# Kernel optimization log

Measured on AMD Instinct MI355X. Metric: run time of the kernel, lower is better.

Reference implementation:

```python
import jax, jax.numpy as jnp
import numpy as np

N = 102400      # total agents across all groups
GROUP = 50      # agents per group
G = N // GROUP  # 2048 groups
E = 128         # embedding_dim
H = 512         # h_dim


def setup_inputs() -> dict:
    key = jax.random.key(0)
    k1, k2, k3, k4, k5, k6 = jax.random.split(key, 6)
    hist_enc = jax.random.normal(k1, (N, H), dtype=jnp.float32)
    hist_pos_batch = jax.random.normal(k2, (N, 2), dtype=jnp.float32)
    # group boundaries: 0, 50, 100, ..., N  (len = G+1)
    seq_start_end = (jnp.arange(G + 1, dtype=jnp.int32) * GROUP)
    # spatial_embedding: Linear(2, E)
    Ws = jax.random.normal(k3, (2, E), dtype=jnp.float32) * (1.0 / np.sqrt(2.0))
    bs = jax.random.normal(k4, (E,), dtype=jnp.float32) * 0.01
    # mlp_pre_pool: Linear(E + H, H)
    Wm = jax.random.normal(k5, (E + H, H), dtype=jnp.float32) * (1.0 / np.sqrt(E + H))
    bm = jax.random.normal(k6, (H,), dtype=jnp.float32) * 0.01
    return {
        "hist_enc": hist_enc,
        "hist_pos_batch": hist_pos_batch,
        "seq_start_end": seq_start_end,
        "Ws": Ws, "bs": bs, "Wm": Wm, "bm": bm,
    }


def reference(hist_enc, hist_pos_batch, seq_start_end, Ws, bs, Wm, bm):
    # The original torch loop builds all n^2 pairs per group but keeps only
    # curr_pool_h[0:1], i.e. row i=0 -> pooled vector for the group's FIRST agent.
    # rel[i=0, j] = pos[j] - pos[start]; hidden index is j; max over j.
    n = hist_enc.shape[0]
    num_groups = seq_start_end.shape[0] - 1
    # segment id of each agent: group g covers [sse[g], sse[g+1])
    seg_ids = jnp.searchsorted(seq_start_end, jnp.arange(n, dtype=seq_start_end.dtype), side="right") - 1
    starts = seq_start_end[:-1]                      # [G]
    anchor = hist_pos_batch[starts][seg_ids]         # [N,2] pos of group's first agent
    rel = hist_pos_batch - anchor                    # [N,2]
    emb = jax.nn.relu(rel @ Ws + bs)                 # [N,E]
    h_in = jnp.concatenate([hist_enc, emb], axis=1)  # [N,E+H]
    pooled = jax.nn.relu(h_in @ Wm + bm)             # [N,H]
    out = jax.ops.segment_max(pooled, seg_ids, num_segments=num_groups)  # [G,H]
    return out
```

## Files before the change

### kernel.cpp

```cpp
#include <hip/hip_runtime.h>


typedef __bf16 bf16x8 __attribute__((ext_vector_type(8)));
typedef float floatx4 __attribute__((ext_vector_type(4)));

constexpr int NR = 102400;
constexpr int NG = 2048;
constexpr int E  = 128;
constexpr int H  = 512;
constexpr int KD = 640;
constexpr int BM = 128, BN = 128, BK = 32;
constexpr int NKT = KD / BK;
constexpr int KH  = H / BK;

__device__ inline unsigned short f2bf(float f) {
    unsigned u = __float_as_uint(f);
    u += 0x7FFF + ((u >> 16) & 1u);
    return (unsigned short)(u >> 16);
}

__device__ inline unsigned pk2(float lo, float hi) {
    return __builtin_amdgcn_perm(__float_as_uint(hi) + 0x8000u,
                                 __float_as_uint(lo) + 0x8000u, 0x07060302u);
}

__device__ inline bf16x8 pk8(float4 a, float4 b) {
    union { uint4 u; bf16x8 v; } c;
    c.u.x = pk2(a.x, a.y); c.u.y = pk2(a.z, a.w);
    c.u.z = pk2(b.x, b.y); c.u.w = pk2(b.z, b.w);
    return c.v;
}

__global__ __launch_bounds__(256) void prep3(
    const float* __restrict__ pos, const int* __restrict__ sse,
    const float* __restrict__ Wm, unsigned short* __restrict__ WmT,
    int* __restrict__ segArr, float* __restrict__ relA)
{
    const int b = blockIdx.x;
    const int t = threadIdx.x;
    __shared__ float tile[64][65];
    if (b < 400) {
        if (!segArr) return;
        const int i = b * 256 + t;
        int l = 0, r = NG + 1;
        while (l < r) { int m = (l + r) >> 1; if (sse[m] <= i) l = m + 1; else r = m; }
        const int g = l - 1;
        segArr[i] = g;
        const int a = sse[g];
        relA[2 * i + 0] = pos[2 * i + 0] - pos[2 * a + 0];
        relA[2 * i + 1] = pos[2 * i + 1] - pos[2 * a + 1];
    } else {
        const int bb = b - 400;
        const int kb = (bb % 10) * 64, nb = (bb / 10) * 64;
        const int tx = t & 63, tq = t >> 6;
#pragma unroll
        for (int i = 0; i < 16; ++i) {
            const int k = tq * 16 + i;
            tile[k][tx] = Wm[(size_t)(kb + k) * H + nb + tx];
        }
        __syncthreads();
#pragma unroll
        for (int i = 0; i < 16; ++i) {
            const int n = tq * 16 + i;
            WmT[(size_t)(nb + n) * KD + kb + tx] = f2bf(tile[tx][n]);
        }
    }
}

__global__ __launch_bounds__(256, 2) void pool_stream(
    const float* __restrict__ hist_enc,
    const int*   __restrict__ sse,
    const int*   __restrict__ segArr,
    const float* __restrict__ relA,
    const float* __restrict__ Ws,
    const float* __restrict__ bs,
    const unsigned short* __restrict__ WmT,
    const float* __restrict__ bm,
    float*       __restrict__ out)
{
    __shared__ __attribute__((aligned(16))) unsigned short Bs[NKT * 64 * 32];

    const int t   = threadIdx.x;
    const int bid = blockIdx.x;
    const int x     = bid & 7;
    const int q     = bid >> 3;
    const int col   = q & 7;
    const int chunk = (q >> 3) * 8 + x;
    const int rowBase = chunk * 256;
    const int cTile   = col * 64;

    const int lane  = t & 63;
    const int wv    = t >> 6;
    const int lcol  = lane & 15;
    const int lquad = lane >> 4;

    {
        const unsigned short* src = WmT + (size_t)cTile * KD;
#pragma unroll
        for (int i = 0; i < 20; ++i) {
            const int idx = i * 256 + t;
            const int r = idx / 80, c8 = idx % 80;
            const uint4 v = *(const uint4*)&src[(size_t)r * KD + c8 * 8];
            const int kt = c8 >> 2;
            const int j  = (c8 & 3) ^ ((r >> 1) & 3);
            *(uint4*)&Bs[kt * 2048 + r * 32 + j * 8] = v;
        }
    }

    const int wbase = rowBase + wv * 64;
    const float* pA[4];
#pragma unroll
    for (int mt = 0; mt < 4; ++mt)
        pA[mt] = hist_enc + (size_t)(wbase + mt * 16 + lcol) * H + lquad * 8;

    float2 relm[4];
#pragma unroll
    for (int mt = 0; mt < 4; ++mt)
        relm[mt] = *(const float2*)&relA[2 * (wbase + mt * 16 + lcol)];

    float bias[4];
#pragma unroll
    for (int nt = 0; nt < 4; ++nt) bias[nt] = bm[cTile + nt * 16 + lcol];

    const int s0 = segArr[wbase];
    const int bA = sse[s0 + 1];
    const int bB = (s0 + 2 <= NG) ? sse[s0 + 2] : 0x7fffffff;

    float4 st[2][4][2];
#pragma unroll
    for (int mt = 0; mt < 4; ++mt) {
        st[0][mt][0] = *(const float4*)(pA[mt] + 0);
        st[0][mt][1] = *(const float4*)(pA[mt] + 4);
        st[1][mt][0] = *(const float4*)(pA[mt] + BK);
        st[1][mt][1] = *(const float4*)(pA[mt] + BK + 4);
    }

    __syncthreads();

    floatx4 acc[4][4];
#pragma unroll
    for (int m = 0; m < 4; ++m)
#pragma unroll
        for (int n = 0; n < 4; ++n) acc[m][n] = (floatx4){0.f, 0.f, 0.f, 0.f};

#pragma unroll
    for (int kt = 0; kt < NKT; ++kt) {
        bf16x8 af[4];
        if (kt < KH) {
#pragma unroll
            for (int mt = 0; mt < 4; ++mt)
                af[mt] = pk8(st[kt & 1][mt][0], st[kt & 1][mt][1]);
            if (kt + 2 < KH) {
#pragma unroll
                for (int mt = 0; mt < 4; ++mt) {
                    st[kt & 1][mt][0] = *(const float4*)(pA[mt] + (kt + 2) * BK);
                    st[kt & 1][mt][1] = *(const float4*)(pA[mt] + (kt + 2) * BK + 4);
                }
            }
        } else {
            const int e0 = (kt - KH) * BK + lquad * 8;
            const float4 w0a = *(const float4*)&Ws[e0];
            const float4 w0b = *(const float4*)&Ws[e0 + 4];
            const float4 w1a = *(const float4*)&Ws[E + e0];
            const float4 w1b = *(const float4*)&Ws[E + e0 + 4];
            const float4 ba4 = *(const float4*)&bs[e0];
            const float4 bb4 = *(const float4*)&bs[e0 + 4];
#pragma unroll
            for (int mt = 0; mt < 4; ++mt) {
                const float r0 = relm[mt].x, r1 = relm[mt].y;
                float4 fa, fb;
                fa.x = fmaxf(r0 * w0a.x + r1 * w1a.x + ba4.x, 0.f);
                fa.y = fmaxf(r0 * w0a.y + r1 * w1a.y + ba4.y, 0.f);
                fa.z = fmaxf(r0 * w0a.z + r1 * w1a.z + ba4.z, 0.f);
                fa.w = fmaxf(r0 * w0a.w + r1 * w1a.w + ba4.w, 0.f);
                fb.x = fmaxf(r0 * w0b.x + r1 * w1b.x + bb4.x, 0.f);
                fb.y = fmaxf(r0 * w0b.y + r1 * w1b.y + bb4.y, 0.f);
                fb.z = fmaxf(r0 * w0b.z + r1 * w1b.z + bb4.z, 0.f);
                fb.w = fmaxf(r0 * w0b.w + r1 * w1b.w + bb4.w, 0.f);
                af[mt] = pk8(fa, fb);
            }
        }

        bf16x8 bfr[4];
#pragma unroll
        for (int nt = 0; nt < 4; ++nt) {
            const int c  = nt * 16 + lcol;
            const int pc = lquad ^ ((c >> 1) & 3);
            bfr[nt] = *(const bf16x8*)&Bs[kt * 2048 + c * 32 + pc * 8];
        }

        __builtin_amdgcn_s_setprio(1);
#pragma unroll
        for (int mt = 0; mt < 4; ++mt)
#pragma unroll
            for (int nt = 0; nt < 4; ++nt)
                acc[mt][nt] = __builtin_amdgcn_mfma_f32_16x16x32_bf16(af[mt], bfr[nt], acc[mt][nt], 0, 0, 0);
        __builtin_amdgcn_s_setprio(0);
    }

    float pm0[4] = {0.f, 0.f, 0.f, 0.f};
    float pm1[4] = {0.f, 0.f, 0.f, 0.f};
    float pm2[4] = {0.f, 0.f, 0.f, 0.f};
#pragma unroll
    for (int nt = 0; nt < 4; ++nt) {
#pragma unroll
        for (int mt = 0; mt < 4; ++mt) {
#pragma unroll
            for (int rr = 0; rr < 4; ++rr) {
                const int rowAbs = wbase + mt * 16 + lquad * 4 + rr;
                const float v = fmaxf(acc[mt][nt][rr] + bias[nt], 0.f);
                const bool geA = rowAbs >= bA;
                const bool geB = rowAbs >= bB;
                pm0[nt] = fmaxf(pm0[nt], (!geA)         ? v : 0.f);
                pm1[nt] = fmaxf(pm1[nt], (geA && !geB)  ? v : 0.f);
                pm2[nt] = fmaxf(pm2[nt], (geB)          ? v : 0.f);
            }
        }
    }
#pragma unroll
    for (int s = 0; s < 3; ++s) {
#pragma unroll
        for (int nt = 0; nt < 4; ++nt) {
            float v = (s == 0) ? pm0[nt] : (s == 1) ? pm1[nt] : pm2[nt];
            v = fmaxf(v, __shfl_xor(v, 16));
            v = fmaxf(v, __shfl_xor(v, 32));
            if (lquad == 0 && v > 0.f) {
                float* dst = &out[(size_t)(s0 + s) * H + cTile + nt * 16 + lcol];
                atomicMax((int*)dst, __float_as_int(v));
            }
        }
    }
}

constexpr int LDAF = 40;
__global__ __launch_bounds__(256) void pool_mfma_fb(
    const float* __restrict__ hist_enc, const float* __restrict__ pos,
    const int* __restrict__ sse, const float* __restrict__ Ws,
    const float* __restrict__ bs, const unsigned short* __restrict__ WmT,
    const float* __restrict__ bm, float* __restrict__ out)
{
    __shared__ __attribute__((aligned(16))) unsigned short As[BM][LDAF];
    __shared__ __attribute__((aligned(16))) unsigned short Bsb[BN][LDAF];
    __shared__ float relRow[BM][2];
    __shared__ int   segRow[BM];
    __shared__ int   bnd[3];
    __shared__ int   Pmax[4][BN + 4];

    const int t = threadIdx.x;
    const int cTile = blockIdx.x * BN;
    const int rowBase = blockIdx.y * BM;

    if (t < BM) {
        const int i = rowBase + t;
        int l = 0, r = NG + 1;
        while (l < r) { int m = (l + r) >> 1; if (sse[m] <= i) l = m + 1; else r = m; }
        const int g = l - 1;
        segRow[t] = g;
        const int a = sse[g];
        relRow[t][0] = pos[2 * i + 0] - pos[2 * a + 0];
        relRow[t][1] = pos[2 * i + 1] - pos[2 * a + 1];
    }
    if (t >= BM && t < BM + 3) bnd[t - BM] = BM;
    for (int idx = t; idx < 4 * (BN + 4); idx += 256) ((int*)Pmax)[idx] = 0;
    __syncthreads();
    if (t < BM - 1) {
        const int s0 = segRow[t], s1 = segRow[t + 1];
        if (s1 != s0) bnd[s1 - segRow[0] - 1] = t + 1;
    }

    const int lane = t & 63, wv = t >> 6;
    const int wr = (wv >> 1) * 64, wc = (wv & 1) * 64;
    const int lcol = lane & 15, lquad = lane >> 4;

    floatx4 acc[4][4];
#pragma unroll
    for (int m = 0; m < 4; ++m)
#pragma unroll
        for (int n = 0; n < 4; ++n) acc[m][n] = (floatx4){0.f, 0.f, 0.f, 0.f};

    for (int kt = 0; kt < KD / BK; ++kt) {
        const int k0 = kt * BK;
        float4 av[4]; uint4 bv[2];
        if (k0 < H) {
#pragma unroll
            for (int i = 0; i < 4; ++i) {
                const int idx = i * 256 + t;
                const int row = idx >> 3, kq = (idx & 7) * 4;
                av[i] = *(const float4*)&hist_enc[(size_t)(rowBase + row) * H + k0 + kq];
            }
        } else {
#pragma unroll
            for (int i = 0; i < 4; ++i) {
                const int idx = i * 256 + t;
                const int row = idx >> 3, kq = (idx & 7) * 4;
                const int e = k0 - H + kq;
                const float4 w0 = *(const float4*)&Ws[e];
                const float4 w1 = *(const float4*)&Ws[E + e];
                const float4 b4 = *(const float4*)&bs[e];
                const float r0 = relRow[row][0], r1 = relRow[row][1];
                av[i].x = fmaxf(r0 * w0.x + r1 * w1.x + b4.x, 0.f);
                av[i].y = fmaxf(r0 * w0.y + r1 * w1.y + b4.y, 0.f);
                av[i].z = fmaxf(r0 * w0.z + r1 * w1.z + b4.z, 0.f);
                av[i].w = fmaxf(r0 * w0.w + r1 * w1.w + b4.w, 0.f);
            }
        }
#pragma unroll
        for (int i = 0; i < 2; ++i) {
            const int idx = i * 256 + t;
            const int n = idx >> 2, q = idx & 3;
            bv[i] = *(const uint4*)&WmT[(size_t)(cTile + n) * KD + k0 + q * 8];
        }
        __syncthreads();
#pragma unroll
        for (int i = 0; i < 4; ++i) {
            const int idx = i * 256 + t;
            const int row = idx >> 3, kq = (idx & 7) * 4;
            ushort4 p;
            p.x = f2bf(av[i].x); p.y = f2bf(av[i].y);
            p.z = f2bf(av[i].z); p.w = f2bf(av[i].w);
            *(ushort4*)&As[row][kq] = p;
        }
#pragma unroll
        for (int i = 0; i < 2; ++i) {
            const int idx = i * 256 + t;
            const int n = idx >> 2, q = idx & 3;
            *(uint4*)&Bsb[n][q * 8] = bv[i];
        }
        __syncthreads();

        bf16x8 af[4], bfr[4];
#pragma unroll
        for (int mt = 0; mt < 4; ++mt)
            af[mt] = *(const bf16x8*)&As[wr + mt * 16 + lcol][lquad * 8];
#pragma unroll
        for (int nt = 0; nt < 4; ++nt)
            bfr[nt] = *(const bf16x8*)&Bsb[wc + nt * 16 + lcol][lquad * 8];
#pragma unroll
        for (int mt = 0; mt < 4; ++mt)
#pragma unroll
            for (int nt = 0; nt < 4; ++nt)
                acc[mt][nt] = __builtin_amdgcn_mfma_f32_16x16x32_bf16(af[mt], bfr[nt], acc[mt][nt], 0, 0, 0);
    }

    const int b0 = bnd[0], b1 = bnd[1], b2 = bnd[2];
    const int segBase = segRow[0];
#pragma unroll
    for (int nt = 0; nt < 4; ++nt) {
        const int col = wc + nt * 16 + lcol;
        const float bias = bm[cTile + col];
        float pm[4] = {0.f, 0.f, 0.f, 0.f};
#pragma unroll
        for (int mt = 0; mt < 4; ++mt) {
#pragma unroll
            for (int r = 0; r < 4; ++r) {
                const int lr = wr + mt * 16 + lquad * 4 + r;
                const int ls = (lr >= b0) + (lr >= b1) + (lr >= b2);
                const float v = fmaxf(acc[mt][nt][r] + bias, 0.f);
                pm[ls] = fmaxf(pm[ls], v);
            }
        }
#pragma unroll
        for (int ls = 0; ls < 4; ++ls)
            if (pm[ls] > 0.f) atomicMax(&Pmax[ls][col], __float_as_int(pm[ls]));
    }
    __syncthreads();
    for (int idx = t; idx < 4 * BN; idx += 256) {
        const int ls = idx >> 7, col = idx & 127;
        if (ls > 0 && bnd[ls - 1] >= BM) continue;
        const int seg = segBase + ls;
        const int v = Pmax[ls][col];
        const int gs = sse[seg], ge = sse[seg + 1];
        float* dst = &out[(size_t)seg * H + cTile + col];
        if (gs >= rowBase && ge <= rowBase + BM) *dst = __int_as_float(v);
        else atomicMax((int*)dst, v);
    }
}

extern "C" void kernel_launch(void* const* d_in, const int* in_sizes, int n_in,
                              void* d_out, int out_size, void* d_ws, size_t ws_size,
                              hipStream_t stream) {
    const float* hist_enc = (const float*)d_in[0];
    const float* pos      = (const float*)d_in[1];
    const int*   sse      = (const int*)  d_in[2];
    const float* Ws       = (const float*)d_in[3];
    const float* bs       = (const float*)d_in[4];
    const float* Wm       = (const float*)d_in[5];
    const float* bm       = (const float*)d_in[6];
    float*       out      = (float*)d_out;

    const size_t needWmT = (size_t)H * KD * 2;
    const size_t needSeg = (size_t)NR * 4;
    const size_t needRel = (size_t)NR * 2 * 4;
    unsigned short* WmT  = (unsigned short*)d_ws;
    int*            segA = (int*)  ((char*)d_ws + needWmT);
    float*          relA = (float*)((char*)d_ws + needWmT + needSeg);

    hipMemsetAsync(out, 0, (size_t)out_size * sizeof(float), stream);

    if (ws_size >= needWmT + needSeg + needRel) {
        prep3<<<480, 256, 0, stream>>>(pos, sse, Wm, WmT, segA, relA);
        pool_stream<<<3200, 256, 0, stream>>>(hist_enc, sse, segA, relA, Ws, bs, WmT, bm, out);
    } else {
        prep3<<<480, 256, 0, stream>>>(pos, sse, Wm, WmT, nullptr, nullptr);
        pool_mfma_fb<<<dim3(H / BN, NR / BM), 256, 0, stream>>>(hist_enc, pos, sse, Ws, bs, WmT, bm, out);
    }
}
```

Before: 444.2 us.

## Flip operand roles: stage activation tile in LDS, stream weights from global

```diff
diff --git a/kernel.cpp b/kernel.cpp
--- a/kernel.cpp
+++ b/kernel.cpp
@@ -22,13 +22,6 @@
 __device__ inline unsigned pk2(float lo, float hi) {
     return __builtin_amdgcn_perm(__float_as_uint(hi) + 0x8000u,
                                  __float_as_uint(lo) + 0x8000u, 0x07060302u);
-}
-
-__device__ inline bf16x8 pk8(float4 a, float4 b) {
-    union { uint4 u; bf16x8 v; } c;
-    c.u.x = pk2(a.x, a.y); c.u.y = pk2(a.z, a.w);
-    c.u.z = pk2(b.x, b.y); c.u.w = pk2(b.z, b.w);
-    return c.v;
 }
 
 __global__ __launch_bounds__(256) void prep3(
@@ -67,7 +60,7 @@
     }
 }
 
-__global__ __launch_bounds__(256, 2) void pool_stream(
+__global__ __launch_bounds__(256, 2) void pool_flip(
     const float* __restrict__ hist_enc,
     const int*   __restrict__ sse,
     const int*   __restrict__ segArr,
@@ -78,115 +71,104 @@
     const float* __restrict__ bm,
     float*       __restrict__ out)
 {
-    __shared__ __attribute__((aligned(16))) unsigned short Bs[NKT * 64 * 32];
+    __shared__ __attribute__((aligned(16))) unsigned short As[NKT * 64 * 32];
 
     const int t   = threadIdx.x;
     const int bid = blockIdx.x;
-    const int x     = bid & 7;
-    const int q     = bid >> 3;
-    const int col   = q & 7;
-    const int chunk = (q >> 3) * 8 + x;
-    const int rowBase = chunk * 256;
-    const int cTile   = col * 64;
+    const int x       = bid & 7;
+    const int r_      = bid >> 3;
+    const int colTile = r_ & 1;
+    const int chunk   = (r_ >> 1) * 8 + x;
+    const int rowBase = chunk * 64;
+    const int cTile   = colTile * 256;
 
     const int lane  = t & 63;
     const int wv    = t >> 6;
     const int lcol  = lane & 15;
     const int lquad = lane >> 4;
+    const int cb    = cTile + wv * 64;
+
+    const unsigned short* pB[4];
+#pragma unroll
+    for (int nt = 0; nt < 4; ++nt)
+        pB[nt] = WmT + (size_t)(cb + nt * 16 + lcol) * KD + lquad * 8;
+
+    uint4 sB[2][4];
+#pragma unroll
+    for (int nt = 0; nt < 4; ++nt) {
+        sB[0][nt] = *(const uint4*)(pB[nt]);
+        sB[1][nt] = *(const uint4*)(pB[nt] + BK);
+    }
 
     {
-        const unsigned short* src = WmT + (size_t)cTile * KD;
-#pragma unroll
-        for (int i = 0; i < 20; ++i) {
-            const int idx = i * 256 + t;
-            const int r = idx / 80, c8 = idx % 80;
-            const uint4 v = *(const uint4*)&src[(size_t)r * KD + c8 * 8];
-            const int kt = c8 >> 2;
-            const int j  = (c8 & 3) ^ ((r >> 1) & 3);
-            *(uint4*)&Bs[kt * 2048 + r * 32 + j * 8] = v;
-        }
-    }
-
-    const int wbase = rowBase + wv * 64;
-    const float* pA[4];
-#pragma unroll
-    for (int mt = 0; mt < 4; ++mt)
-        pA[mt] = hist_enc + (size_t)(wbase + mt * 16 + lcol) * H + lquad * 8;
-
-    float2 relm[4];
-#pragma unroll
-    for (int mt = 0; mt < 4; ++mt)
-        relm[mt] = *(const float2*)&relA[2 * (wbase + mt * 16 + lcol)];
-
-    float bias[4];
-#pragma unroll
-    for (int nt = 0; nt < 4; ++nt) bias[nt] = bm[cTile + nt * 16 + lcol];
-
-    const int s0 = segArr[wbase];
-    const int bA = sse[s0 + 1];
-    const int bB = (s0 + 2 <= NG) ? sse[s0 + 2] : 0x7fffffff;
-
-    float4 st[2][4][2];
-#pragma unroll
-    for (int mt = 0; mt < 4; ++mt) {
-        st[0][mt][0] = *(const float4*)(pA[mt] + 0);
-        st[0][mt][1] = *(const float4*)(pA[mt] + 4);
-        st[1][mt][0] = *(const float4*)(pA[mt] + BK);
-        st[1][mt][1] = *(const float4*)(pA[mt] + BK + 4);
-    }
-
-    __syncthreads();
-
-    floatx4 acc[4][4];
-#pragma unroll
-    for (int m = 0; m < 4; ++m)
-#pragma unroll
-        for (int n = 0; n < 4; ++n) acc[m][n] = (floatx4){0.f, 0.f, 0.f, 0.f};
-
-#pragma unroll
-    for (int kt = 0; kt < NKT; ++kt) {
-        bf16x8 af[4];
-        if (kt < KH) {
-#pragma unroll
-            for (int mt = 0; mt < 4; ++mt)
-                af[mt] = pk8(st[kt & 1][mt][0], st[kt & 1][mt][1]);
-            if (kt + 2 < KH) {
-#pragma unroll
-                for (int mt = 0; mt < 4; ++mt) {
-                    st[kt & 1][mt][0] = *(const float4*)(pA[mt] + (kt + 2) * BK);
-                    st[kt & 1][mt][1] = *(const float4*)(pA[mt] + (kt + 2) * BK + 4);
-                }
-            }
-        } else {
-            const int e0 = (kt - KH) * BK + lquad * 8;
+        const int row  = t >> 2;
+        const int phys = t & 3;
+        const int swz  = (row >> 1) & 3;
+        const float* src = hist_enc + (size_t)(rowBase + row) * H + phys * 8;
+#pragma unroll
+        for (int i = 0; i < 16; ++i) {
+            const float4 f0 = *(const float4*)(src + i * 32);
+            const float4 f1 = *(const float4*)(src + i * 32 + 4);
+            uint4 u;
+            u.x = pk2(f0.x, f0.y); u.y = pk2(f0.z, f0.w);
+            u.z = pk2(f1.x, f1.y); u.w = pk2(f1.z, f1.w);
+            *(uint4*)&As[i * 2048 + row * 32 + (phys ^ swz) * 8] = u;
+        }
+        const float2 rr = *(const float2*)&relA[2 * (size_t)(rowBase + row)];
+#pragma unroll
+        for (int i = 0; i < 4; ++i) {
+            const int e0 = (phys + 4 * i) * 8;
             const float4 w0a = *(const float4*)&Ws[e0];
             const float4 w0b = *(const float4*)&Ws[e0 + 4];
             const float4 w1a = *(const float4*)&Ws[E + e0];
             const float4 w1b = *(const float4*)&Ws[E + e0 + 4];
             const float4 ba4 = *(const float4*)&bs[e0];
             const float4 bb4 = *(const float4*)&bs[e0 + 4];
-#pragma unroll
-            for (int mt = 0; mt < 4; ++mt) {
-                const float r0 = relm[mt].x, r1 = relm[mt].y;
-                float4 fa, fb;
-                fa.x = fmaxf(r0 * w0a.x + r1 * w1a.x + ba4.x, 0.f);
-                fa.y = fmaxf(r0 * w0a.y + r1 * w1a.y + ba4.y, 0.f);
-                fa.z = fmaxf(r0 * w0a.z + r1 * w1a.z + ba4.z, 0.f);
-                fa.w = fmaxf(r0 * w0a.w + r1 * w1a.w + ba4.w, 0.f);
-                fb.x = fmaxf(r0 * w0b.x + r1 * w1b.x + bb4.x, 0.f);
-                fb.y = fmaxf(r0 * w0b.y + r1 * w1b.y + bb4.y, 0.f);
-                fb.z = fmaxf(r0 * w0b.z + r1 * w1b.z + bb4.z, 0.f);
-                fb.w = fmaxf(r0 * w0b.w + r1 * w1b.w + bb4.w, 0.f);
-                af[mt] = pk8(fa, fb);
-            }
-        }
-
+            float4 fa, fb;
+            fa.x = fmaxf(rr.x * w0a.x + rr.y * w1a.x + ba4.x, 0.f);
+            fa.y = fmaxf(rr.x * w0a.y + rr.y * w1a.y + ba4.y, 0.f);
+            fa.z = fmaxf(rr.x * w0a.z + rr.y * w1a.z + ba4.z, 0.f);
+            fa.w = fmaxf(rr.x * w0a.w + rr.y * w1a.w + ba4.w, 0.f);
+            fb.x = fmaxf(rr.x * w0b.x + rr.y * w1b.x + bb4.x, 0.f);
+            fb.y = fmaxf(rr.x * w0b.y + rr.y * w1b.y + bb4.y, 0.f);
+            fb.z = fmaxf(rr.x * w0b.z + rr.y * w1b.z + bb4.z, 0.f);
+            fb.w = fmaxf(rr.x * w0b.w + rr.y * w1b.w + bb4.w, 0.f);
+            uint4 u;
+            u.x = pk2(fa.x, fa.y); u.y = pk2(fa.z, fa.w);
+            u.z = pk2(fb.x, fb.y); u.w = pk2(fb.z, fb.w);
+            *(uint4*)&As[(16 + i) * 2048 + row * 32 + (phys ^ swz) * 8] = u;
+        }
+    }
+
+    float bias[4];
+#pragma unroll
+    for (int nt = 0; nt < 4; ++nt) bias[nt] = bm[cb + nt * 16 + lcol];
+    const int s0 = segArr[rowBase];
+    const int bA = sse[s0 + 1];
+    const int bB = (s0 + 2 <= NG) ? sse[s0 + 2] : 0x7fffffff;
+
+    __syncthreads();
+
+    floatx4 acc[4][4];
+#pragma unroll
+    for (int m = 0; m < 4; ++m)
+#pragma unroll
+        for (int n = 0; n < 4; ++n) acc[m][n] = (floatx4){0.f, 0.f, 0.f, 0.f};
+
+#pragma unroll
+    for (int kt = 0; kt < NKT; ++kt) {
+        bf16x8 af[4];
+#pragma unroll
+        for (int mt = 0; mt < 4; ++mt) {
+            const int R  = mt * 16 + lcol;
+            const int pc = lquad ^ ((R >> 1) & 3);
+            af[mt] = *(const bf16x8*)&As[kt * 2048 + R * 32 + pc * 8];
+        }
         bf16x8 bfr[4];
 #pragma unroll
         for (int nt = 0; nt < 4; ++nt) {
-            const int c  = nt * 16 + lcol;
-            const int pc = lquad ^ ((c >> 1) & 3);
-            bfr[nt] = *(const bf16x8*)&Bs[kt * 2048 + c * 32 + pc * 8];
+            union { uint4 u; bf16x8 v; } c; c.u = sB[kt & 1][nt];
+            bfr[nt] = c.v;
         }
 
         __builtin_amdgcn_s_setprio(1);
@@ -196,6 +178,12 @@
             for (int nt = 0; nt < 4; ++nt)
                 acc[mt][nt] = __builtin_amdgcn_mfma_f32_16x16x32_bf16(af[mt], bfr[nt], acc[mt][nt], 0, 0, 0);
         __builtin_amdgcn_s_setprio(0);
+
+        if (kt + 2 < NKT) {
+#pragma unroll
+            for (int nt = 0; nt < 4; ++nt)
+                sB[kt & 1][nt] = *(const uint4*)(pB[nt] + (kt + 2) * BK);
+        }
     }
 
     float pm0[4] = {0.f, 0.f, 0.f, 0.f};
@@ -207,13 +195,13 @@
         for (int mt = 0; mt < 4; ++mt) {
 #pragma unroll
             for (int rr = 0; rr < 4; ++rr) {
-                const int rowAbs = wbase + mt * 16 + lquad * 4 + rr;
+                const int rowAbs = rowBase + mt * 16 + lquad * 4 + rr;
                 const float v = fmaxf(acc[mt][nt][rr] + bias[nt], 0.f);
                 const bool geA = rowAbs >= bA;
                 const bool geB = rowAbs >= bB;
-                pm0[nt] = fmaxf(pm0[nt], (!geA)         ? v : 0.f);
-                pm1[nt] = fmaxf(pm1[nt], (geA && !geB)  ? v : 0.f);
-                pm2[nt] = fmaxf(pm2[nt], (geB)          ? v : 0.f);
+                pm0[nt] = fmaxf(pm0[nt], (!geA)        ? v : 0.f);
+                pm1[nt] = fmaxf(pm1[nt], (geA && !geB) ? v : 0.f);
+                pm2[nt] = fmaxf(pm2[nt], (geB)         ? v : 0.f);
             }
         }
     }
@@ -225,7 +213,7 @@
             v = fmaxf(v, __shfl_xor(v, 16));
             v = fmaxf(v, __shfl_xor(v, 32));
             if (lquad == 0 && v > 0.f) {
-                float* dst = &out[(size_t)(s0 + s) * H + cTile + nt * 16 + lcol];
+                float* dst = &out[(size_t)(s0 + s) * H + cb + nt * 16 + lcol];
                 atomicMax((int*)dst, __float_as_int(v));
             }
         }
@@ -239,7 +227,7 @@
     const float* __restrict__ bs, const unsigned short* __restrict__ WmT,
     const float* __restrict__ bm, float* __restrict__ out)
 {
-    __shared__ __attribute__((aligned(16))) unsigned short As[BM][LDAF];
+    __shared__ __attribute__((aligned(16))) unsigned short Asf[BM][LDAF];
     __shared__ __attribute__((aligned(16))) unsigned short Bsb[BN][LDAF];
     __shared__ float relRow[BM][2];
     __shared__ int   segRow[BM];
@@ -318,7 +306,7 @@
             ushort4 p;
             p.x = f2bf(av[i].x); p.y = f2bf(av[i].y);
             p.z = f2bf(av[i].z); p.w = f2bf(av[i].w);
-            *(ushort4*)&As[row][kq] = p;
+            *(ushort4*)&Asf[row][kq] = p;
         }
 #pragma unroll
         for (int i = 0; i < 2; ++i) {
@@ -331,7 +319,7 @@
         bf16x8 af[4], bfr[4];
 #pragma unroll
         for (int mt = 0; mt < 4; ++mt)
-            af[mt] = *(const bf16x8*)&As[wr + mt * 16 + lcol][lquad * 8];
+            af[mt] = *(const bf16x8*)&Asf[wr + mt * 16 + lcol][lquad * 8];
 #pragma unroll
         for (int nt = 0; nt < 4; ++nt)
             bfr[nt] = *(const bf16x8*)&Bsb[wc + nt * 16 + lcol][lquad * 8];
@@ -399,7 +387,7 @@
 
     if (ws_size >= needWmT + needSeg + needRel) {
         prep3<<<480, 256, 0, stream>>>(pos, sse, Wm, WmT, segA, relA);
-        pool_stream<<<3200, 256, 0, stream>>>(hist_enc, sse, segA, relA, Ws, bs, WmT, bm, out);
+        pool_flip<<<3200, 256, 0, stream>>>(hist_enc, sse, segA, relA, Ws, bs, WmT, bm, out);
     } else {
         prep3<<<480, 256, 0, stream>>>(pos, sse, Wm, WmT, nullptr, nullptr);
         pool_mfma_fb<<<dim3(H / BN, NR / BM), 256, 0, stream>>>(hist_enc, pos, sse, Ws, bs, WmT, bm, out);
```

Measured after the change: 409.9 us. 1.08x faster.
